# Kernel tuning notes

Hardware: AMD Instinct MI355X
Metric: run time of the kernel (lower is better)

Reference implementation:

```python
import jax, jax.numpy as jnp
import numpy as np

DIM = 512
HEADS = 8
DIM_HEAD = 64
LANDMARKS = 256
PINV_ITERS = 6
RES_K = 33


def layernorm(x, g, b, eps=1e-5):
    mu = jnp.mean(x, -1, keepdims=True)
    var = jnp.mean((x - mu) ** 2, -1, keepdims=True)
    return (x - mu) / jnp.sqrt(var + eps) * g + b


def moore_penrose_pinv(x, iters=PINV_ITERS):
    abs_x = jnp.abs(x)
    col = abs_x.sum(-1)
    row = abs_x.sum(-2)
    z = jnp.swapaxes(x, -1, -2) / (jnp.max(col) * jnp.max(row))
    I = jnp.eye(x.shape[-1], dtype=x.dtype)
    for _ in range(iters):
        xz = x @ z
        z = 0.25 * z @ (13.0 * I - xz @ (15.0 * I - xz @ (7.0 * I - xz)))
    return z


def nystrom_attention(x, Wqkv, Wout, bout, res_w):
    b, n, _ = x.shape
    m = LANDMARKS
    pad = (m - n % m) % m
    if pad:
        x = jnp.pad(x, ((0, 0), (pad, 0), (0, 0)))  # front pad, as in lucidrains impl
    qkv = x @ Wqkv  # (b, np, 3*inner)
    q, k, v = jnp.split(qkv, 3, axis=-1)
    to_heads = lambda t: t.reshape(b, -1, HEADS, DIM_HEAD).transpose(0, 2, 1, 3)
    q, k, v = to_heads(q), to_heads(k), to_heads(v)  # (b,h,np,d)
    q = q * (DIM_HEAD ** -0.5)
    l = -(-n // m)  # ceil(n/m), tokens per landmark
    ql = q.reshape(b, HEADS, m, l, DIM_HEAD).sum(3) / l  # (b,h,m,d)
    kl = k.reshape(b, HEADS, m, l, DIM_HEAD).sum(3) / l
    sim1 = jnp.einsum('bhid,bhjd->bhij', q, kl)   # (b,h,np,m)
    sim2 = jnp.einsum('bhid,bhjd->bhij', ql, kl)  # (b,h,m,m)
    sim3 = jnp.einsum('bhid,bhjd->bhij', ql, k)   # (b,h,m,np)
    a1 = jax.nn.softmax(sim1, -1)
    a2 = jax.nn.softmax(sim2, -1)
    a3 = jax.nn.softmax(sim3, -1)
    a2_inv = moore_penrose_pinv(a2)
    out = (a1 @ a2_inv) @ (a3 @ v)  # (b,h,np,d)
    # depthwise residual conv along sequence (kernel 33x1, groups=heads, no bias)
    res = jax.lax.conv_general_dilated(
        v, res_w, (1, 1), [(RES_K // 2, RES_K // 2), (0, 0)],
        dimension_numbers=('NCHW', 'OIHW', 'NCHW'), feature_group_count=HEADS)
    out = out + res
    out = out.transpose(0, 2, 1, 3).reshape(b, -1, HEADS * DIM_HEAD)
    out = out @ Wout + bout
    return out[:, -n:]


def depthwise2d(x, w, b, pad):
    y = jax.lax.conv_general_dilated(
        x, w, (1, 1), [(pad, pad), (pad, pad)],
        dimension_numbers=('NCHW', 'OIHW', 'NCHW'), feature_group_count=DIM)
    return y + b[None, :, None, None]


def ppeg(x, H, W, w7, b7, w5, b5, w3, b3):
    B, _, C = x.shape
    cls_tok, feat = x[:, :1], x[:, 1:]
    cnn = feat.transpose(0, 2, 1).reshape(B, C, H, W)
    y = depthwise2d(cnn, w7, b7, 3) + cnn + depthwise2d(cnn, w5, b5, 2) + depthwise2d(cnn, w3, b3, 1)
    y = y.reshape(B, C, H * W).transpose(0, 2, 1)
    return jnp.concatenate([cls_tok, y], axis=1)


def setup_inputs() -> dict:
    key = jax.random.key(0)
    ks = jax.random.split(key, 20)
    s = 0.02
    n_classes = 5
    inp = {
        'data': jax.random.normal(ks[0], (1, 15000, 1024), jnp.float32),
        'W_fc1': jax.random.normal(ks[1], (1024, DIM), jnp.float32) * s,
        'b_fc1': jnp.zeros((DIM,), jnp.float32),
        'cls_token': jax.random.normal(ks[2], (1, 1, DIM), jnp.float32),
        'ln1_g': jnp.ones((DIM,), jnp.float32), 'ln1_b': jnp.zeros((DIM,), jnp.float32),
        'qkv1': jax.random.normal(ks[3], (DIM, 3 * HEADS * DIM_HEAD), jnp.float32) * s,
        'out1_w': jax.random.normal(ks[4], (HEADS * DIM_HEAD, DIM), jnp.float32) * s,
        'out1_b': jnp.zeros((DIM,), jnp.float32),
        'res1': jax.random.normal(ks[5], (HEADS, 1, RES_K, 1), jnp.float32) * s,
        'w7': jax.random.normal(ks[6], (DIM, 1, 7, 7), jnp.float32) * s,
        'b7': jnp.zeros((DIM,), jnp.float32),
        'w5': jax.random.normal(ks[7], (DIM, 1, 5, 5), jnp.float32) * s,
        'b5': jnp.zeros((DIM,), jnp.float32),
        'w3': jax.random.normal(ks[8], (DIM, 1, 3, 3), jnp.float32) * s,
        'b3': jnp.zeros((DIM,), jnp.float32),
        'ln2_g': jnp.ones((DIM,), jnp.float32), 'ln2_b': jnp.zeros((DIM,), jnp.float32),
        'qkv2': jax.random.normal(ks[9], (DIM, 3 * HEADS * DIM_HEAD), jnp.float32) * s,
        'out2_w': jax.random.normal(ks[10], (HEADS * DIM_HEAD, DIM), jnp.float32) * s,
        'out2_b': jnp.zeros((DIM,), jnp.float32),
        'res2': jax.random.normal(ks[11], (HEADS, 1, RES_K, 1), jnp.float32) * s,
        'norm_g': jnp.ones((DIM,), jnp.float32), 'norm_b': jnp.zeros((DIM,), jnp.float32),
        'W_fc2': jax.random.normal(ks[12], (DIM, n_classes), jnp.float32) * s,
        'b_fc2': jnp.zeros((n_classes,), jnp.float32),
    }
    return inp


def reference(data, W_fc1, b_fc1, cls_token, ln1_g, ln1_b, qkv1, out1_w, out1_b, res1,
              w7, b7, w5, b5, w3, b3, ln2_g, ln2_b, qkv2, out2_w, out2_b, res2,
              norm_g, norm_b, W_fc2, b_fc2):
    h = jax.nn.relu(data @ W_fc1 + b_fc1)  # (B, N, 512)
    N = h.shape[1]
    _H = int(np.ceil(np.sqrt(N)))
    _W = _H
    add = _H * _W - N
    h = jnp.concatenate([h, h[:, :add]], axis=1)  # pad to square grid
    B = h.shape[0]
    h = jnp.concatenate([jnp.broadcast_to(cls_token, (B, 1, DIM)), h], axis=1)
    h = h + nystrom_attention(layernorm(h, ln1_g, ln1_b), qkv1, out1_w, out1_b, res1)
    h = ppeg(h, _H, _W, w7, b7, w5, b5, w3, b3)
    h = h + nystrom_attention(layernorm(h, ln2_g, ln2_b), qkv2, out2_w, out2_b, res2)
    h = layernorm(h, norm_g, norm_b)[:, 0]
    logits = h @ W_fc2 + b_fc2
    Y_prob = jax.nn.softmax(logits, -1)
    Y_hat = jnp.argmax(logits, -1)
    return logits, Y_prob, Y_hat
```

## Files before the change

kernel.cpp:

```cpp
#include <hip/hip_runtime.h>
#include <math.h>

#define NP 15360
#define NPQ 15488
#define NTOK 15130
#define HG 123

typedef __attribute__((ext_vector_type(8))) short s8b;
typedef __attribute__((ext_vector_type(4))) float f4;

__device__ inline float bf2f(ushort u) { return __uint_as_float(((unsigned)u) << 16); }
__device__ inline ushort f2bf(float f) {
    unsigned u = __float_as_uint(f);
    unsigned r = (u + 0x7fffu + ((u >> 16) & 1u)) >> 16;
    return (ushort)r;
}

__global__ __launch_bounds__(256)
void gemm_f32(const float* __restrict__ A, int lda, long sA,
              const float* __restrict__ B, int ldb, long sB,
              float* __restrict__ C, int ldc, long sC,
              int M, int N, int K,
              const float* __restrict__ bias,
              const float* __restrict__ E, int ldE, long sE, float eS,
              float cS, int relu, int accum)
{
    A += (long)blockIdx.z * sA;
    B += (long)blockIdx.z * sB;
    C += (long)blockIdx.z * sC;
    if (E) E += (long)blockIdx.z * sE;
    const int m0 = blockIdx.y * 64, n0 = blockIdx.x * 64;
    const int t = threadIdx.x;
    const int tx = t & 15, ty = t >> 4;
    __shared__ float As[16][64];
    __shared__ float Bs[16][64];
    float acc[4][4] = {};
    const int arow = t >> 2, akc = (t & 3) * 4;
    const int brow = t >> 4, bnc = (t & 15) * 4;
    for (int k0 = 0; k0 < K; k0 += 16) {
        float4 av = make_float4(0.f, 0.f, 0.f, 0.f);
        if (m0 + arow < M) av = *(const float4*)(A + (long)(m0 + arow) * lda + k0 + akc);
        As[akc + 0][arow] = av.x; As[akc + 1][arow] = av.y;
        As[akc + 2][arow] = av.z; As[akc + 3][arow] = av.w;
        float4 bv = *(const float4*)(B + (long)(k0 + brow) * ldb + n0 + bnc);
        *(float4*)&Bs[brow][bnc] = bv;
        __syncthreads();
#pragma unroll
        for (int kk = 0; kk < 16; ++kk) {
            float4 a4 = *(const float4*)&As[kk][ty * 4];
            float4 b4 = *(const float4*)&Bs[kk][tx * 4];
            float a[4] = {a4.x, a4.y, a4.z, a4.w};
            float b[4] = {b4.x, b4.y, b4.z, b4.w};
#pragma unroll
            for (int i = 0; i < 4; i++)
#pragma unroll
                for (int j = 0; j < 4; j++) acc[i][j] = fmaf(a[i], b[j], acc[i][j]);
        }
        __syncthreads();
    }
#pragma unroll
    for (int i = 0; i < 4; i++) {
        int m = m0 + ty * 4 + i;
        if (m < M) {
#pragma unroll
            for (int j = 0; j < 4; j++) {
                int n = n0 + tx * 4 + j;
                float v = cS * acc[i][j];
                if (E) v = fmaf(eS, E[(long)m * ldE + n], v);
                if (bias) v += bias[n];
                if (relu) v = fmaxf(v, 0.f);
                if (accum) C[(long)m * ldc + n] += v;
                else C[(long)m * ldc + n] = v;
            }
        }
    }
}

template<int MT, int NT, int WROWS, int WCOLS>
__global__ __launch_bounds__(256)
void gemm_mfma(const ushort* __restrict__ A, int lda, long sA,
               const ushort* __restrict__ Bt, int ldb, long sB,
               float* __restrict__ C, int ldc, long sC,
               int M, int K,
               const float* __restrict__ bias, int relu, int accum)
{
    constexpr int TM = MT * 16 * WROWS;
    constexpr int TN = NT * 16 * WCOLS;
    constexpr int BKP = 40;
    constexpr int AIT = TM / 64;
    constexpr int BIT = TN / 64;
    __shared__ ushort As[TM * BKP];
    __shared__ ushort Bs[TN * BKP];
    A  += (long)blockIdx.z * sA;
    Bt += (long)blockIdx.z * sB;
    C  += (long)blockIdx.z * sC;
    const int t = threadIdx.x;
    const int nwg = gridDim.x * gridDim.y;
    const int flat = blockIdx.y * gridDim.x + blockIdx.x;
    const int q8 = nwg >> 3, r8 = nwg & 7;
    const int xcd = flat & 7, idx = flat >> 3;
    const int swz = (xcd < r8) ? (xcd * (q8 + 1) + idx)
                               : (r8 * (q8 + 1) + (xcd - r8) * q8 + idx);
    const int m0 = (swz / gridDim.x) * TM;
    const int n0 = (swz % gridDim.x) * TN;
    const int w = t >> 6, l = t & 63;
    const int wm = (w / WCOLS) * (MT * 16), wn = (w % WCOLS) * (NT * 16);
    const int lr = l & 15;
    const int lk = (l >> 4) * 8;
    const int srow = t >> 2, skc = (t & 3) * 8;
    f4 acc[MT][NT] = {};
    s8b pa[AIT], pb[BIT];
#pragma unroll
    for (int i = 0; i < AIT; i++)
        pa[i] = *(const s8b*)(A + (long)(m0 + srow + i * 64) * lda + skc);
#pragma unroll
    for (int i = 0; i < BIT; i++)
        pb[i] = *(const s8b*)(Bt + (long)(n0 + srow + i * 64) * ldb + skc);
    for (int k0 = 0; k0 < K; k0 += 32) {
        __syncthreads();
#pragma unroll
        for (int i = 0; i < AIT; i++)
            *(s8b*)(&As[(srow + i * 64) * BKP + skc]) = pa[i];
#pragma unroll
        for (int i = 0; i < BIT; i++)
            *(s8b*)(&Bs[(srow + i * 64) * BKP + skc]) = pb[i];
        if (k0 + 32 < K) {
#pragma unroll
            for (int i = 0; i < AIT; i++)
                pa[i] = *(const s8b*)(A + (long)(m0 + srow + i * 64) * lda + k0 + 32 + skc);
#pragma unroll
            for (int i = 0; i < BIT; i++)
                pb[i] = *(const s8b*)(Bt + (long)(n0 + srow + i * 64) * ldb + k0 + 32 + skc);
        }
        __syncthreads();
        s8b af[MT], bf[NT];
#pragma unroll
        for (int i = 0; i < MT; i++) af[i] = *(const s8b*)(&As[(wm + i * 16 + lr) * BKP + lk]);
#pragma unroll
        for (int j = 0; j < NT; j++) bf[j] = *(const s8b*)(&Bs[(wn + j * 16 + lr) * BKP + lk]);
#pragma unroll
        for (int i = 0; i < MT; i++)
#pragma unroll
            for (int j = 0; j < NT; j++)
                acc[i][j] = __builtin_amdgcn_mfma_f32_16x16x32_bf16(af[i], bf[j], acc[i][j], 0, 0, 0);
    }
    const int orow = (l >> 4) * 4;
#pragma unroll
    for (int i = 0; i < MT; i++) {
#pragma unroll
        for (int r = 0; r < 4; r++) {
            int m = m0 + wm + i * 16 + orow + r;
            if (m < M) {
#pragma unroll
                for (int j = 0; j < NT; j++) {
                    int n = n0 + wn + j * 16 + lr;
                    float vv = acc[i][j][r];
                    if (bias) vv += bias[n];
                    if (relu) vv = fmaxf(vv, 0.f);
                    if (accum) C[(long)m * ldc + n] += vv;
                    else C[(long)m * ldc + n] = vv;
                }
            }
        }
    }
}

__global__ __launch_bounds__(256)
void gemm_nn16(const ushort* __restrict__ A, const ushort* __restrict__ B,
               const ushort* __restrict__ E, ushort* __restrict__ C,
               int N, int K, float cS, float eS, long sAB)
{
    __shared__ ushort As[64 * 40];
    __shared__ ushort Bs[64 * 40];
    A += (long)blockIdx.z * sAB;
    B += (long)blockIdx.z * sAB;
    if (E) E += (long)blockIdx.z * sAB;
    C += (long)blockIdx.z * sAB;
    const int t = threadIdx.x;
    const int m0 = blockIdx.y * 64, n0 = blockIdx.x * 64;
    const int w = t >> 6, l = t & 63;
    const int wm = (w >> 1) * 32, wn = (w & 1) * 32;
    const int lr = l & 15, lk = (l >> 4) * 8;
    const int quad = l >> 4;
    const int arow = t >> 2, akc = (t & 3) * 8;
    const int bkk = t >> 3, bnc = (t & 7) * 8;
    const int bcolp = (bkk + ((bnc >> 3) & 3) * 8) & 31;
    f4 acc[2][2] = {};
    s8b pa = *(const s8b*)(A + (long)(m0 + arow) * K + akc);
    s8b pb = *(const s8b*)(B + (long)bkk * N + n0 + bnc);
    for (int k0 = 0; k0 < K; k0 += 32) {
        __syncthreads();
        *(s8b*)(&As[arow * 40 + akc]) = pa;
#pragma unroll
        for (int j = 0; j < 8; j++) Bs[(bnc + j) * 40 + bcolp] = ((ushort*)&pb)[j];
        if (k0 + 32 < K) {
            pa = *(const s8b*)(A + (long)(m0 + arow) * K + k0 + 32 + akc);
            pb = *(const s8b*)(B + (long)(k0 + 32 + bkk) * N + n0 + bnc);
        }
        __syncthreads();
        s8b af[2], bf[2];
#pragma unroll
        for (int i = 0; i < 2; i++) af[i] = *(const s8b*)(&As[(wm + i * 16 + lr) * 40 + lk]);
#pragma unroll
        for (int j = 0; j < 2; j++) {
            int n = wn + j * 16 + lr;
            int cb = ((quad + ((n >> 3) & 3)) & 3) * 8;
            bf[j] = *(const s8b*)(&Bs[n * 40 + cb]);
        }
#pragma unroll
        for (int i = 0; i < 2; i++)
#pragma unroll
            for (int j = 0; j < 2; j++)
                acc[i][j] = __builtin_amdgcn_mfma_f32_16x16x32_bf16(af[i], bf[j], acc[i][j], 0, 0, 0);
    }
    const int orow = (l >> 4) * 4;
#pragma unroll
    for (int i = 0; i < 2; i++)
#pragma unroll
        for (int r = 0; r < 4; r++) {
            int m = m0 + wm + i * 16 + orow + r;
#pragma unroll
            for (int j = 0; j < 2; j++) {
                int n = wn + j * 16 + lr;
                float vv = cS * acc[i][j][r];
                if (E) vv = fmaf(eS, bf2f(E[(long)m * N + n0 + n]), vv);
                C[(long)m * N + n0 + n] = f2bf(vv);
            }
        }
}

__global__ __launch_bounds__(256)
void gemm_qkv_mfma(const ushort* __restrict__ A, const ushort* __restrict__ Bt,
                   ushort* __restrict__ qo, ushort* __restrict__ ko, ushort* __restrict__ vo)
{
    constexpr int BKP = 40;
    __shared__ ushort As[128 * BKP];
    __shared__ ushort Bs[128 * BKP];
    const int t = threadIdx.x;
    const int nwg = gridDim.x * gridDim.y;
    const int flat = blockIdx.y * gridDim.x + blockIdx.x;
    const int q8 = nwg >> 3, r8 = nwg & 7;
    const int xcd = flat & 7, idx = flat >> 3;
    const int swz = (xcd < r8) ? (xcd * (q8 + 1) + idx)
                               : (r8 * (q8 + 1) + (xcd - r8) * q8 + idx);
    const int m0 = (swz / gridDim.x) * 128;
    const int n0 = (swz % gridDim.x) * 128;
    const int w = t >> 6, l = t & 63;
    const int wm = (w >> 1) * 64, wn = (w & 1) * 64;
    const int lr = l & 15;
    const int lk = (l >> 4) * 8;
    const int srow = t >> 2, skc = (t & 3) * 8;
    f4 acc[4][4] = {};
    s8b pa[2], pb[2];
#pragma unroll
    for (int i = 0; i < 2; i++) {
        pa[i] = *(const s8b*)(A + (long)(m0 + srow + i * 64) * 512 + skc);
        pb[i] = *(const s8b*)(Bt + (long)(n0 + srow + i * 64) * 512 + skc);
    }
    for (int k0 = 0; k0 < 512; k0 += 32) {
        __syncthreads();
#pragma unroll
        for (int i = 0; i < 2; i++) {
            *(s8b*)(&As[(srow + i * 64) * BKP + skc]) = pa[i];
            *(s8b*)(&Bs[(srow + i * 64) * BKP + skc]) = pb[i];
        }
        if (k0 + 32 < 512) {
#pragma unroll
            for (int i = 0; i < 2; i++) {
                pa[i] = *(const s8b*)(A + (long)(m0 + srow + i * 64) * 512 + k0 + 32 + skc);
                pb[i] = *(const s8b*)(Bt + (long)(n0 + srow + i * 64) * 512 + k0 + 32 + skc);
            }
        }
        __syncthreads();
        s8b af[4], bf[4];
#pragma unroll
        for (int i = 0; i < 4; i++) af[i] = *(const s8b*)(&As[(wm + i * 16 + lr) * BKP + lk]);
#pragma unroll
        for (int j = 0; j < 4; j++) bf[j] = *(const s8b*)(&Bs[(wn + j * 16 + lr) * BKP + lk]);
#pragma unroll
        for (int i = 0; i < 4; i++)
#pragma unroll
            for (int j = 0; j < 4; j++)
                acc[i][j] = __builtin_amdgcn_mfma_f32_16x16x32_bf16(af[i], bf[j], acc[i][j], 0, 0, 0);
    }
    const int orow = (l >> 4) * 4;
#pragma unroll
    for (int i = 0; i < 4; i++) {
#pragma unroll
        for (int r = 0; r < 4; r++) {
            int m = m0 + wm + i * 16 + orow + r;
#pragma unroll
            for (int j = 0; j < 4; j++) {
                int col = n0 + wn + j * 16 + lr;
                int which = col >> 9, h = (col >> 6) & 7, d = col & 63;
                float vv = acc[i][j][r];
                if (which == 0) vv *= 0.125f;
                ushort* dst = which == 0 ? qo : (which == 1 ? ko : vo);
                dst[((long)h * NPQ + m) * 64 + d] = f2bf(vv);
            }
        }
    }
}

__global__ __launch_bounds__(256, 3)
void k_flash_a3v(const ushort* __restrict__ qlb, const ushort* __restrict__ kg,
                 const ushort* __restrict__ vg,
                 float* __restrict__ pacc, float* __restrict__ pml)
{
    const int c = blockIdx.x;
    const int qt = blockIdx.y;
    const int h = blockIdx.z;
    const int t = threadIdx.x;
    const int w = t >> 6, lane = t & 63;
    const int quad = lane >> 4, l16 = lane & 15;
    const s8b vones = {0x3F80, 0x3F80, 0x3F80, 0x3F80, 0x3F80, 0x3F80, 0x3F80, 0x3F80};

    __shared__ union {
        struct { ushort Vt[64][40]; ushort Ps[128][40]; } s;
        float Os[128][68];
    } L;

    s8b aq[2][2];
    const ushort* qbase = qlb + ((long)h * 256 + qt * 128 + w * 32) * 64;
#pragma unroll
    for (int mi = 0; mi < 2; mi++)
#pragma unroll
        for (int kf = 0; kf < 2; kf++)
            aq[mi][kf] = *(const s8b*)(qbase + (mi * 16 + l16) * 64 + kf * 32 + quad * 8);

    f4 oacc[2][4] = {};
    f4 lacc[2] = {};

    const ushort* kh = kg + (long)h * NPQ * 64;
    const ushort* vh = vg + (long)h * NPQ * 64;
    const int key0c = c * 256;

    const int vkk = (t >> 3) & 31;
    const int vdc = (t & 7) * 8;
    const int vcolp = (vkk + ((vdc >> 3) & 3) * 8) & 31;

    s8b vvN = *(const s8b*)(vh + (long)(key0c + vkk) * 64 + vdc);
    s8b bqN[2][2];
#pragma unroll
    for (int nj = 0; nj < 2; nj++)
#pragma unroll
        for (int kf = 0; kf < 2; kf++)
            bqN[nj][kf] = *(const s8b*)(kh + (long)(key0c + nj * 16 + l16) * 64 + kf * 32 + quad * 8);

#pragma unroll
    for (int sub = 0; sub < 8; sub++) {
        int key0 = key0c + sub * 32;
        s8b vvC = vvN;
        s8b bq[2][2];
#pragma unroll
        for (int nj = 0; nj < 2; nj++)
#pragma unroll
            for (int kf = 0; kf < 2; kf++) bq[nj][kf] = bqN[nj][kf];
        if (sub < 7) {
            vvN = *(const s8b*)(vh + (long)(key0 + 32 + vkk) * 64 + vdc);
#pragma unroll
            for (int nj = 0; nj < 2; nj++)
#pragma unroll
                for (int kf = 0; kf < 2; kf++)
                    bqN[nj][kf] = *(const s8b*)(kh + (long)(key0 + 32 + nj * 16 + l16) * 64 + kf * 32 + quad * 8);
        }
        __syncthreads();
        {
#pragma unroll
            for (int j = 0; j < 8; j++) L.s.Vt[vdc + j][vcolp] = ((ushort*)&vvC)[j];
        }
        f4 sacc[2][2] = {};
#pragma unroll
        for (int mi = 0; mi < 2; mi++)
#pragma unroll
            for (int nj = 0; nj < 2; nj++) {
                sacc[mi][nj] = __builtin_amdgcn_mfma_f32_16x16x32_bf16(aq[mi][0], bq[nj][0], sacc[mi][nj], 0, 0, 0);
                sacc[mi][nj] = __builtin_amdgcn_mfma_f32_16x16x32_bf16(aq[mi][1], bq[nj][1], sacc[mi][nj], 0, 0, 0);
            }
#pragma unroll
        for (int mi = 0; mi < 2; mi++)
#pragma unroll
            for (int r = 0; r < 4; r++) {
                int row = w * 32 + mi * 16 + quad * 4 + r;
                L.s.Ps[row][l16]      = f2bf(__expf(sacc[mi][0][r]));
                L.s.Ps[row][16 + l16] = f2bf(__expf(sacc[mi][1][r]));
            }
        __syncthreads();
        s8b ap[2], bv[4];
#pragma unroll
        for (int mi = 0; mi < 2; mi++)
            ap[mi] = *(const s8b*)(&L.s.Ps[w * 32 + mi * 16 + l16][quad * 8]);
#pragma unroll
        for (int dj = 0; dj < 4; dj++) {
            int d = dj * 16 + l16;
            int rot = (d >> 3) & 3;
            int cb = ((quad + rot) & 3) * 8;
            bv[dj] = *(const s8b*)(&L.s.Vt[d][cb]);
        }
#pragma unroll
        for (int mi = 0; mi < 2; mi++) {
#pragma unroll
            for (int dj = 0; dj < 4; dj++)
                oacc[mi][dj] = __builtin_amdgcn_mfma_f32_16x16x32_bf16(ap[mi], bv[dj], oacc[mi][dj], 0, 0, 0);
            lacc[mi] = __builtin_amdgcn_mfma_f32_16x16x32_bf16(ap[mi], vones, lacc[mi], 0, 0, 0);
        }
    }
    __syncthreads();
#pragma unroll
    for (int mi = 0; mi < 2; mi++)
#pragma unroll
        for (int dj = 0; dj < 4; dj++)
#pragma unroll
            for (int r = 0; r < 4; r++)
                L.Os[w * 32 + mi * 16 + quad * 4 + r][dj * 16 + l16] = oacc[mi][dj][r];
    long pbase = (long)(h * 60 + c);
    if (l16 == 0) {
#pragma unroll
        for (int mi = 0; mi < 2; mi++)
#pragma unroll
            for (int r = 0; r < 4; r++) {
                int i = qt * 128 + w * 32 + mi * 16 + quad * 4 + r;
                pml[pbase * 512 + i] = 0.f;
                pml[pbase * 512 + 256 + i] = lacc[mi][r];
            }
    }
    __syncthreads();
    float* pc = pacc + pbase * 16384 + qt * 128;
    int d = t >> 2, ig = t & 3;
#pragma unroll
    for (int u = 0; u < 8; u++) {
        int i0 = ig * 32 + u * 4;
        float4 v4 = make_float4(L.Os[i0][d], L.Os[i0 + 1][d], L.Os[i0 + 2][d], L.Os[i0 + 3][d]);
        *(float4*)(pc + (long)d * 256 + i0) = v4;
    }
}

__global__ __launch_bounds__(256, 3)
void k_attn1(const ushort* __restrict__ qg, const ushort* __restrict__ klb,
             const ushort* __restrict__ BmT, const ushort* __restrict__ vg,
             const float* __restrict__ rw, ushort* __restrict__ ohb)
{
    const int m0 = blockIdx.x * 128;
    const int h = blockIdx.y;
    const int t = threadIdx.x;
    const int w = t >> 6, lane = t & 63;
    const int quad = lane >> 4, l16 = lane & 15;
    const s8b vones = {0x3F80, 0x3F80, 0x3F80, 0x3F80, 0x3F80, 0x3F80, 0x3F80, 0x3F80};

    __shared__ union {
        ushort Ps[2][128][40];
        ushort Os[128][68];
    } L;
    __shared__ __attribute__((aligned(16))) ushort Vs[160][64];

    const ushort* vh = vg + (long)h * NPQ * 64;
    {
        const ushort* srcw = vh + (long)(214 + m0 + w * 40) * 64 + lane * 8;
        ushort* dstw = &Vs[w * 40][0];
#pragma unroll
        for (int it = 0; it < 5; it++)
            __builtin_amdgcn_global_load_lds(
                (const __attribute__((address_space(1))) void*)(srcw + it * 512),
                (__attribute__((address_space(3))) void*)(dstw + it * 512),
                16, 0, 0);
    }

    s8b aq[2][2];
    const ushort* qbase = qg + ((long)h * NPQ + 230 + m0 + w * 32) * 64;
#pragma unroll
    for (int mi = 0; mi < 2; mi++)
#pragma unroll
        for (int kf = 0; kf < 2; kf++)
            aq[mi][kf] = *(const s8b*)(qbase + (mi * 16 + l16) * 64 + kf * 32 + quad * 8);

    const ushort* kh = klb + (long)h * 16384;
    const ushort* bmt = BmT + (long)h * 16384;

    s8b bqN[2][2];
#pragma unroll
    for (int nj = 0; nj < 2; nj++)
#pragma unroll
        for (int kf = 0; kf < 2; kf++)
            bqN[nj][kf] = *(const s8b*)(kh + (long)(nj * 16 + l16) * 64 + kf * 32 + quad * 8);

    f4 oacc[2][4] = {};
    f4 lacc[2] = {};
#pragma unroll
    for (int sub = 0; sub < 8; sub++) {
        int key0 = sub * 32;
        s8b bq[2][2];
#pragma unroll
        for (int nj = 0; nj < 2; nj++)
#pragma unroll
            for (int kf = 0; kf < 2; kf++) bq[nj][kf] = bqN[nj][kf];
        if (sub < 7) {
#pragma unroll
            for (int nj = 0; nj < 2; nj++)
#pragma unroll
                for (int kf = 0; kf < 2; kf++)
                    bqN[nj][kf] = *(const s8b*)(kh + (long)(key0 + 32 + nj * 16 + l16) * 64 + kf * 32 + quad * 8);
        }
        s8b bv[4];
#pragma unroll
        for (int dj = 0; dj < 4; dj++)
            bv[dj] = *(const s8b*)(bmt + (long)(dj * 16 + l16) * 256 + key0 + quad * 8);
        f4 sacc[2][2] = {};
#pragma unroll
        for (int mi = 0; mi < 2; mi++)
#pragma unroll
            for (int nj = 0; nj < 2; nj++) {
                sacc[mi][nj] = __builtin_amdgcn_mfma_f32_16x16x32_bf16(aq[mi][0], bq[nj][0], sacc[mi][nj], 0, 0, 0);
                sacc[mi][nj] = __builtin_amdgcn_mfma_f32_16x16x32_bf16(aq[mi][1], bq[nj][1], sacc[mi][nj], 0, 0, 0);
            }
        int par = sub & 1;
#pragma unroll
        for (int mi = 0; mi < 2; mi++)
#pragma unroll
            for (int r = 0; r < 4; r++) {
                int row = w * 32 + mi * 16 + quad * 4 + r;
                L.Ps[par][row][l16]      = f2bf(__expf(sacc[mi][0][r]));
                L.Ps[par][row][16 + l16] = f2bf(__expf(sacc[mi][1][r]));
            }
        s8b ap[2];
#pragma unroll
        for (int mi = 0; mi < 2; mi++)
            ap[mi] = *(const s8b*)(&L.Ps[par][w * 32 + mi * 16 + l16][quad * 8]);
#pragma unroll
        for (int mi = 0; mi < 2; mi++) {
#pragma unroll
            for (int dj = 0; dj < 4; dj++)
                oacc[mi][dj] = __builtin_amdgcn_mfma_f32_16x16x32_bf16(ap[mi], bv[dj], oacc[mi][dj], 0, 0, 0);
            lacc[mi] = __builtin_amdgcn_mfma_f32_16x16x32_bf16(ap[mi], vones, lacc[mi], 0, 0, 0);
        }
    }
    __syncthreads();

    if (214 + m0 + 160 > NP) {
        for (int r = w * 32; r < w * 32 + 64 && r < 160; ++r)
            if (214 + m0 + r >= NP) Vs[r][lane] = 0;
    }

#pragma unroll
    for (int mi = 0; mi < 2; mi++)
#pragma unroll
        for (int r = 0; r < 4; r++) {
            float inv = 1.f / lacc[mi][r];
            int row = w * 32 + mi * 16 + quad * 4 + r;
#pragma unroll
            for (int dj = 0; dj < 4; dj++)
                L.Os[row][dj * 16 + l16] = f2bf(oacc[mi][dj][r] * inv);
        }
    float rwf[33];
#pragma unroll
    for (int kk = 0; kk < 33; kk++) rwf[kk] = rw[h * 33 + kk];
#pragma unroll
    for (int half = 0; half < 2; half++) {
        const int rbase = w * 32 + half * 16;
        float vr[48];
#pragma unroll
        for (int s = 0; s < 48; s++) vr[s] = bf2f(Vs[rbase + s][lane]);
        float conv[16];
#pragma unroll
        for (int i = 0; i < 16; i++) conv[i] = 0.f;
#pragma unroll
        for (int kk = 0; kk < 33; kk++) {
            float wk = rwf[kk];
#pragma unroll
            for (int i = 0; i < 16; i++) conv[i] = fmaf(wk, vr[i + kk], conv[i]);
        }
        int t0 = m0 + rbase;
#pragma unroll
        for (int i = 0; i < 16; i++) {
            int tk = t0 + i;
            if (tk < NTOK) {
                float val = bf2f(L.Os[rbase + i][lane]) + conv[i];
                ohb[(long)tk * 512 + h * 64 + lane] = f2bf(val);
            }
        }
    }
}

__global__ __launch_bounds__(256)
void k_layernorm(const float* __restrict__ h, ushort* __restrict__ xln,
                 const float* __restrict__ g, const float* __restrict__ b, int pad)
{
    int row = blockIdx.x, t = threadIdx.x;
    if (row < pad) {
        xln[(long)row * 512 + t] = 0;
        xln[(long)row * 512 + t + 256] = 0;
        return;
    }
    const float* src = h + (long)(row - pad) * 512;
    float x1 = src[t], x2 = src[t + 256];
    float s = x1 + x2, q = x1 * x1 + x2 * x2;
    __shared__ float rs[4], rq[4], st[2];
    int wid = t >> 6, lane = t & 63;
#pragma unroll
    for (int o = 32; o > 0; o >>= 1) { s += __shfl_down(s, o); q += __shfl_down(q, o); }
    if (lane == 0) { rs[wid] = s; rq[wid] = q; }
    __syncthreads();
    if (t == 0) {
        float S = rs[0] + rs[1] + rs[2] + rs[3];
        float Q = rq[0] + rq[1] + rq[2] + rq[3];
        float mean = S / 512.f;
        float var = Q / 512.f - mean * mean;
        st[0] = mean; st[1] = rsqrtf(var + 1e-5f);
    }
    __syncthreads();
    float mean = st[0], rstd = st[1];
    xln[(long)row * 512 + t] = f2bf((x1 - mean) * rstd * g[t] + b[t]);
    xln[(long)row * 512 + t + 256] = f2bf((x2 - mean) * rstd * g[t + 256] + b[t + 256]);
}

__global__ __launch_bounds__(256)
void k_padcls(float* __restrict__ hbuf, const float* __restrict__ cls)
{
    int i = blockIdx.x, t = threadIdx.x;
    if (i == 0) { hbuf[t] = cls[t]; hbuf[t + 256] = cls[t + 256]; }
    else {
        hbuf[(long)(15000 + i) * 512 + t] = hbuf[(long)i * 512 + t];
        hbuf[(long)(15000 + i) * 512 + t + 256] = hbuf[(long)i * 512 + t + 256];
    }
}

__global__ __launch_bounds__(256)
void k_wT(const float* __restrict__ Wm, ushort* __restrict__ Wt, int K, int N, long sW, long sWt)
{
    Wm += (long)blockIdx.z * sW; Wt += (long)blockIdx.z * sWt;
    __shared__ float tile[32][33];
    int tx = threadIdx.x & 31, ty = threadIdx.x >> 5;
    int n0 = blockIdx.x * 32, k0 = blockIdx.y * 32;
#pragma unroll
    for (int u = 0; u < 4; u++) tile[ty + u * 8][tx] = Wm[(long)(k0 + ty + u * 8) * N + n0 + tx];
    __syncthreads();
#pragma unroll
    for (int u = 0; u < 4; u++) Wt[(long)(n0 + ty + u * 8) * K + k0 + tx] = f2bf(tile[tx][ty + u * 8]);
}

__global__ __launch_bounds__(256)
void k_cvt(const float4* __restrict__ src, ushort4* __restrict__ dst, long n4)
{
    long i = (long)blockIdx.x * 256 + threadIdx.x;
    if (i < n4) {
        float4 v = src[i];
        ushort4 o;
        o.x = f2bf(v.x); o.y = f2bf(v.y); o.z = f2bf(v.z); o.w = f2bf(v.w);
        dst[i] = o;
    }
}

__global__ __launch_bounds__(256)
void k_b2f(const ushort4* __restrict__ src, float4* __restrict__ dst, long n4)
{
    long i = (long)blockIdx.x * 256 + threadIdx.x;
    if (i < n4) {
        ushort4 v = src[i];
        dst[i] = make_float4(bf2f(v.x), bf2f(v.y), bf2f(v.z), bf2f(v.w));
    }
}

__global__ __launch_bounds__(64)
void k_landmarks(const ushort* __restrict__ q, const ushort* __restrict__ k,
                 float* __restrict__ ql, ushort* __restrict__ qlb,
                 float* __restrict__ klT, ushort* __restrict__ klb,
                 unsigned* __restrict__ scal)
{
    int i = blockIdx.x, h = blockIdx.y, d = threadIdx.x;
    if (i == 0 && h == 0 && d == 0) { scal[0] = 0u; scal[1] = 0u; }
    long base = ((long)h * NPQ + (long)i * 60) * 64 + d;
    float sq = 0.f, sk = 0.f;
    for (int j = 0; j < 60; j++) { sq += bf2f(q[base + j * 64]); sk += bf2f(k[base + j * 64]); }
    float qv = sq / 60.f, kv = sk / 60.f;
    ql[((long)h * 256 + i) * 64 + d] = qv;
    qlb[((long)h * 256 + i) * 64 + d] = f2bf(qv);
    klT[((long)h * 64 + d) * 256 + i] = kv;
    klb[((long)h * 256 + i) * 64 + d] = f2bf(kv);
}

__global__ __launch_bounds__(256)
void k_softmax256(float* __restrict__ X, ushort* __restrict__ X16, long headStride)
{
    float* row = X + (long)blockIdx.y * headStride + (long)blockIdx.x * 256;
    int t = threadIdx.x, wid = t >> 6, lane = t & 63;
    float x = row[t];
    __shared__ float rm[4], rsum[4], fin[2];
    float m = x;
#pragma unroll
    for (int o = 32; o > 0; o >>= 1) m = fmaxf(m, __shfl_down(m, o));
    if (lane == 0) rm[wid] = m;
    __syncthreads();
    if (t == 0) fin[0] = fmaxf(fmaxf(rm[0], rm[1]), fmaxf(rm[2], rm[3]));
    __syncthreads();
    float e = __expf(x - fin[0]);
    float s = e;
#pragma unroll
    for (int o = 32; o > 0; o >>= 1) s += __shfl_down(s, o);
    if (lane == 0) rsum[wid] = s;
    __syncthreads();
    if (t == 0) fin[1] = rsum[0] + rsum[1] + rsum[2] + rsum[3];
    __syncthreads();
    float v = e / fin[1];
    row[t] = v;
    if (X16) X16[(long)blockIdx.y * headStride + (long)blockIdx.x * 256 + t] = f2bf(v);
}

__global__ __launch_bounds__(256)
void k_colmax(const float* __restrict__ a2, unsigned* __restrict__ scal)
{
    int h = blockIdx.x, t = threadIdx.x, wid = t >> 6, lane = t & 63;
    const float* A = a2 + (long)h * 65536;
    float cs = 0.f, rs = 0.f;
    for (int i = 0; i < 256; i++) cs += A[(long)i * 256 + t];
    for (int j = 0; j < 256; j++) rs += A[(long)t * 256 + j];
    __shared__ float r1[4], r2[4];
    float m1v = cs, m2v = rs;
#pragma unroll
    for (int o = 32; o > 0; o >>= 1) {
        m1v = fmaxf(m1v, __shfl_down(m1v, o));
        m2v = fmaxf(m2v, __shfl_down(m2v, o));
    }
    if (lane == 0) { r1[wid] = m1v; r2[wid] = m2v; }
    __syncthreads();
    if (t == 0) {
        float a = fmaxf(fmaxf(r1[0], r1[1]), fmaxf(r1[2], r1[3]));
        float b = fmaxf(fmaxf(r2[0], r2[1]), fmaxf(r2[2], r2[3]));
        atomicMax(scal + 0, __float_as_uint(a));
        atomicMax(scal + 1, __float_as_uint(b));
    }
}

__global__ __launch_bounds__(256)
void k_zinit(const float* __restrict__ a2, ushort* __restrict__ zb, const unsigned* __restrict__ scal)
{
    float s = 1.f / (__uint_as_float(scal[0]) * __uint_as_float(scal[1]));
    const float* A = a2 + (long)blockIdx.z * 65536;
    ushort* Z = zb + (long)blockIdx.z * 65536;
    __shared__ float tile[32][33];
    int tx = threadIdx.x & 31, ty = threadIdx.x >> 5;
    int i0 = blockIdx.x * 32, j0 = blockIdx.y * 32;
#pragma unroll
    for (int u = 0; u < 4; u++) tile[ty + u * 8][tx] = A[(long)(j0 + ty + u * 8) * 256 + i0 + tx];
    __syncthreads();
#pragma unroll
    for (int u = 0; u < 4; u++) Z[(long)(i0 + ty + u * 8) * 256 + j0 + tx] = f2bf(tile[tx][ty + u * 8] * s);
}

__global__ __launch_bounds__(256)
void k_a3v_merge(const float* __restrict__ pacc, const float* __restrict__ pml,
                 float* __restrict__ t1)
{
    int d = blockIdx.x, h = blockIdx.y, i = threadIdx.x;
    float M = -INFINITY, L = 0.f, num = 0.f;
    for (int c = 0; c < 60; c++) {
        float mc = pml[(long)(h * 60 + c) * 2 * 256 + i];
        float lc = pml[((long)(h * 60 + c) * 2 + 1) * 256 + i];
        float ac = pacc[((long)(h * 60 + c) * 64 + d) * 256 + i];
        if (mc > M) {
            float f = __expf(M - mc);
            num = num * f + ac; L = L * f + lc; M = mc;
        } else {
            float p = __expf(mc - M);
            num = fmaf(p, ac, num); L = fmaf(p, lc, L);
        }
    }
    t1[((long)h * 256 + i) * 64 + d] = num / L;
}

__global__ __launch_bounds__(256)
void k_cls(const ushort* __restrict__ qb, const float* __restrict__ klT,
           const float* __restrict__ Bm, const ushort* __restrict__ vb,
           const float* __restrict__ rw, float* __restrict__ oh)
{
    int h = blockIdx.x, t = threadIdx.x, wid = t >> 6, lane = t & 63;
    __shared__ float qs[64], p[256], red[256];
    __shared__ float rm[4], rsum[4], fin[2];
    if (t < 64) qs[t] = bf2f(qb[((long)h * NPQ + 230) * 64 + t]);
    __syncthreads();
    float s = 0.f;
    for (int d = 0; d < 64; d++) s = fmaf(qs[d], klT[((long)h * 64 + d) * 256 + t], s);
    float m = s;
#pragma unroll
    for (int o = 32; o > 0; o >>= 1) m = fmaxf(m, __shfl_down(m, o));
    if (lane == 0) rm[wid] = m;
    __syncthreads();
    if (t == 0) fin[0] = fmaxf(fmaxf(rm[0], rm[1]), fmaxf(rm[2], rm[3]));
    __syncthreads();
    float e = __expf(s - fin[0]);
    float ss = e;
#pragma unroll
    for (int o = 32; o > 0; o >>= 1) ss += __shfl_down(ss, o);
    if (lane == 0) rsum[wid] = ss;
    __syncthreads();
    if (t == 0) fin[1] = rsum[0] + rsum[1] + rsum[2] + rsum[3];
    __syncthreads();
    p[t] = e / fin[1];
    __syncthreads();
    int d = t & 63, grp = t >> 6;
    float o = 0.f;
    for (int j = grp * 64; j < grp * 64 + 64; j++) o = fmaf(p[j], Bm[((long)h * 256 + j) * 64 + d], o);
    red[t] = o;
    __syncthreads();
    if (t < 64) {
        float val = red[t] + red[t + 64] + red[t + 128] + red[t + 192];
#pragma unroll
        for (int kk = 0; kk < 33; kk++)
            val = fmaf(rw[h * 33 + kk], bf2f(vb[((long)h * NPQ + 214 + kk) * 64 + t]), val);
        oh[h * 64 + t] = val;
    }
}

__global__ __launch_bounds__(256)
void k_copy4(const float4* __restrict__ src, float4* __restrict__ dst, long n4)
{
    long i = (long)blockIdx.x * 256 + threadIdx.x;
    if (i < n4) dst[i] = src[i];
}

__global__ __launch_bounds__(512)
void k_wcomb(const float* __restrict__ w7, const float* __restrict__ b7,
             const float* __restrict__ w5, const float* __restrict__ b5,
             const float* __restrict__ w3, const float* __restrict__ b3,
             float* __restrict__ wc, float* __restrict__ bc)
{
    int k = blockIdx.x, c = threadIdx.x;
    int kr = k / 7, kc = k % 7;
    float v = w7[c * 49 + k];
    if (kr >= 1 && kr <= 5 && kc >= 1 && kc <= 5) v += w5[c * 25 + (kr - 1) * 5 + (kc - 1)];
    if (kr >= 2 && kr <= 4 && kc >= 2 && kc <= 4) v += w3[c * 9 + (kr - 2) * 3 + (kc - 2)];
    if (k == 24) v += 1.f;
    wc[k * 512 + c] = v;
    if (k == 0) bc[c] = b7[c] + b5[c] + b3[c];
}

__global__ __launch_bounds__(256, 4)
void k_ppeg4(const float* __restrict__ cnn, float* __restrict__ hbuf,
             const float* __restrict__ wc, const float* __restrict__ bc)
{
    __shared__ __attribute__((aligned(16))) float tile[320 * 32];
    const int t = threadIdx.x;
    const int w = t >> 6, lane = t & 63;
    const int c0 = blockIdx.x * 16;
    const int r0 = blockIdx.y * 8;
    const int cb = blockIdx.z * 32;
    {
        const int pl = lane >> 3;
        const int c4 = (lane & 7) * 4;
#pragma unroll
        for (int it = 0; it < 10; ++it) {
            int chunk = w * 10 + it;
            int pos = chunk * 8 + pl;
            int pr = pos / 22, pc = pos - pr * 22;
            int gr = r0 + pr - 3, gc = c0 + pc - 3;
            int grc = min(max(gr, 0), HG - 1), gcc = min(max(gc, 0), HG - 1);
            const float* src = cnn + (long)(grc * HG + gcc) * 512 + cb + c4;
            __builtin_amdgcn_global_load_lds(
                (const __attribute__((address_space(1))) void*)src,
                (__attribute__((address_space(3))) void*)(tile + chunk * 256),
                16, 0, 0);
        }
    }
    __syncthreads();
    const bool boundary = (r0 < 3) | (r0 > HG - 11) | (c0 < 3) | (c0 > HG - 19);
    if (boundary) {
        for (int pos = t; pos < 308; pos += 256) {
            int pr = pos / 22, pc = pos - pr * 22;
            int gr = r0 + pr - 3, gc = c0 + pc - 3;
            if (gr < 0 || gr >= HG || gc < 0 || gc >= HG) {
                float4 z = make_float4(0.f, 0.f, 0.f, 0.f);
#pragma unroll
                for (int c4 = 0; c4 < 32; c4 += 4) *(float4*)&tile[pos * 32 + c4] = z;
            }
        }
        __syncthreads();
    }
    const int cp = t & 15;
    const int slot = t >> 4;
    const int orow = slot >> 1;
    const int ohalf = (slot & 1) * 8;
    float a0[8], a1[8];
#pragma unroll
    for (int i = 0; i < 8; i++) { a0[i] = 0.f; a1[i] = 0.f; }
    for (int kr = 0; kr < 7; kr++) {
        float w0[14], w1[14];
        const float* trow = tile + ((orow + kr) * 22 + ohalf) * 32 + cp * 2;
#pragma unroll
        for (int j = 0; j < 14; j++) {
            float2 v = *(const float2*)(trow + j * 32);
            w0[j] = v.x; w1[j] = v.y;
        }
#pragma unroll
        for (int kc = 0; kc < 7; kc++) {
            float2 wv = *(const float2*)(wc + (long)(kr * 7 + kc) * 512 + cb + cp * 2);
#pragma unroll
            for (int i = 0; i < 8; i++) {
                a0[i] = fmaf(wv.x, w0[i + kc], a0[i]);
                a1[i] = fmaf(wv.y, w1[i + kc], a1[i]);
            }
        }
    }
    const float2 bv = *(const float2*)(bc + cb + cp * 2);
    const int gr = r0 + orow;
    if (gr < HG) {
#pragma unroll
        for (int i = 0; i < 8; i++) {
            int gc = c0 + ohalf + i;
            if (gc < HG) {
                float* dst = hbuf + (long)(1 + gr * HG + gc) * 512 + cb + cp * 2;
                dst[0] = a0[i] + bv.x;
                dst[1] = a1[i] + bv.y;
            }
        }
    }
}

__global__ __launch_bounds__(256)
void k_final(const float* __restrict__ hbuf, const float* __restrict__ g,
             const float* __restrict__ b, const float* __restrict__ W2,
             const float* __restrict__ b2, float* __restrict__ out)
{
    __shared__ float y[512];
    __shared__ float rs[4], rq[4], st[2], lg[8];
    int t = threadIdx.x, wid = t >> 6, lane = t & 63;
    float x1 = hbuf[t], x2 = hbuf[t + 256];
    float s = x1 + x2, q = x1 * x1 + x2 * x2;
#pragma unroll
    for (int o = 32; o > 0; o >>= 1) { s += __shfl_down(s, o); q += __shfl_down(q, o); }
    if (lane == 0) { rs[wid] = s; rq[wid] = q; }
    __syncthreads();
    if (t == 0) {
        float S = rs[0] + rs[1] + rs[2] + rs[3];
        float Q = rq[0] + rq[1] + rq[2] + rq[3];
        float mean = S / 512.f;
        float var = Q / 512.f - mean * mean;
        st[0] = mean; st[1] = rsqrtf(var + 1e-5f);
    }
    __syncthreads();
    float mean = st[0], rstd = st[1];
    y[t] = (x1 - mean) * rstd * g[t] + b[t];
    y[t + 256] = (x2 - mean) * rstd * g[t + 256] + b[t + 256];
    __syncthreads();
    if (t < 5) {
        float acc = b2[t];
        for (int kx = 0; kx < 512; kx++) acc = fmaf(y[kx], W2[kx * 5 + t], acc);
        lg[t] = acc;
    }
    __syncthreads();
    if (t == 0) {
        float mx = lg[0]; int am = 0;
        for (int j = 1; j < 5; j++) if (lg[j] > mx) { mx = lg[j]; am = j; }
        float e[5], se = 0.f;
        for (int j = 0; j < 5; j++) { e[j] = __expf(lg[j] - mx); se += e[j]; }
        for (int j = 0; j < 5; j++) { out[j] = lg[j]; out[5 + j] = e[j] / se; }
        out[10] = (float)am;
    }
}

extern "C" void kernel_launch(void* const* d_in, const int* in_sizes, int n_in,
                              void* d_out, int out_size, void* d_ws, size_t ws_size,
                              hipStream_t stream)
{
    const float* data  = (const float*)d_in[0];
    const float* Wfc1  = (const float*)d_in[1];
    const float* bfc1  = (const float*)d_in[2];
    const float* cls   = (const float*)d_in[3];
    const float* ln1g  = (const float*)d_in[4];
    const float* ln1b  = (const float*)d_in[5];
    const float* qkv1  = (const float*)d_in[6];
    const float* out1w = (const float*)d_in[7];
    const float* out1b = (const float*)d_in[8];
    const float* res1  = (const float*)d_in[9];
    const float* w7    = (const float*)d_in[10];
    const float* b7    = (const float*)d_in[11];
    const float* w5    = (const float*)d_in[12];
    const float* b5    = (const float*)d_in[13];
    const float* w3    = (const float*)d_in[14];
    const float* b3    = (const float*)d_in[15];
    const float* ln2g  = (const float*)d_in[16];
    const float* ln2b  = (const float*)d_in[17];
    const float* qkv2  = (const float*)d_in[18];
    const float* out2w = (const float*)d_in[19];
    const float* out2b = (const float*)d_in[20];
    const float* res2  = (const float*)d_in[21];
    const float* normg = (const float*)d_in[22];
    const float* normb = (const float*)d_in[23];
    const float* Wfc2  = (const float*)d_in[24];
    const float* bfc2  = (const float*)d_in[25];
    float* out = (float*)d_out;

    float* W = (float*)d_ws;
    size_t off = 0;
    auto alloc = [&](size_t n) { size_t o = off; off += (n + 255) & ~(size_t)255; return o; };
    float*  hbuf   = W + alloc((size_t)NTOK * 512);
    float*  ohreg  = W + alloc((size_t)15232 * 512);
    float*  oh     = ohreg;
    ushort* xln    = (ushort*)ohreg;
    ushort* qb16   = (ushort*)(W + alloc((size_t)8 * NPQ * 32));
    ushort* kb16   = (ushort*)(W + alloc((size_t)8 * NPQ * 32));
    ushort* vb16   = (ushort*)(W + alloc((size_t)8 * NPQ * 32));
    float*  ql     = W + alloc(8 * 256 * 64);
    ushort* qlb    = (ushort*)(W + alloc(8 * 256 * 32));
    float*  klT    = W + alloc(8 * 64 * 256);
    ushort* klb    = (ushort*)(W + alloc(8 * 256 * 32));
    float*  a2     = W + alloc(8 * 65536);
    ushort* a2b    = (ushort*)(W + alloc(8 * 32768));
    ushort* zb0    = (ushort*)(W + alloc(8 * 32768));
    ushort* zb1    = (ushort*)(W + alloc(8 * 32768));
    ushort* m1b    = (ushort*)(W + alloc(8 * 32768));
    ushort* mab    = (ushort*)(W + alloc(8 * 32768));
    ushort* mbb    = (ushort*)(W + alloc(8 * 32768));
    float*  z0     = W + alloc(8 * 65536);
    float*  t1     = W + alloc(8 * 256 * 64);
    float*  Bm     = W + alloc(8 * 256 * 64);
    ushort* BmbT   = (ushort*)(W + alloc(8 * 256 * 32));
    float*  scal   = W + alloc(64);
    ushort* ohb16  = (ushort*)(W + alloc((size_t)15232 * 256));
    ushort* WfcT   = (ushort*)(W + alloc(1024 * 256));
    ushort* qkv1T  = (ushort*)(W + alloc(1536 * 256));
    ushort* qkv2T  = (ushort*)(W + alloc(1536 * 256));
    ushort* out1T  = (ushort*)(W + alloc(512 * 256));
    ushort* out2T  = (ushort*)(W + alloc(512 * 256));
    float*  wc     = W + alloc(49 * 512);
    float*  bc     = W + alloc(512);
    float*  big    = W + alloc(8110080);
    ushort* datab  = (ushort*)big;
    float*  pacc   = big;
    float*  pml    = big + 7864320;
    float*  cnn    = big;
    if (ws_size < off * sizeof(float)) return;

    k_wT<<<dim3(16, 32, 1), 256, 0, stream>>>(Wfc1, WfcT, 1024, 512, 0, 0);
    k_wT<<<dim3(48, 16, 1), 256, 0, stream>>>(qkv1, qkv1T, 512, 1536, 0, 0);
    k_wT<<<dim3(48, 16, 1), 256, 0, stream>>>(qkv2, qkv2T, 512, 1536, 0, 0);
    k_wT<<<dim3(16, 16, 1), 256, 0, stream>>>(out1w, out1T, 512, 512, 0, 0);
    k_wT<<<dim3(16, 16, 1), 256, 0, stream>>>(out2w, out2T, 512, 512, 0, 0);
    k_wcomb<<<49, 512, 0, stream>>>(w7, b7, w5, b5, w3, b3, wc, bc);
    k_cvt<<<15000, 256, 0, stream>>>((const float4*)data, (ushort4*)datab, 3840000);
    gemm_mfma<2, 4, 2, 2><<<dim3(4, 235, 1), 256, 0, stream>>>(
        datab, 1024, 0, WfcT, 1024, 0, hbuf + 512, 512, 0, 15000, 1024, bfc1, 1, 0);
    k_padcls<<<130, 256, 0, stream>>>(hbuf, cls);

    auto layer = [&](const float* lng, const float* lnb, const ushort* qkvT,
                     const float* outW, const ushort* outT, const float* outB,
                     const float* resW, bool full) {
        k_layernorm<<<NP, 256, 0, stream>>>(hbuf, xln, lng, lnb, 230);
        gemm_qkv_mfma<<<dim3(12, 120, 1), 256, 0, stream>>>(xln, qkvT, qb16, kb16, vb16);
        k_landmarks<<<dim3(256, 8), 64, 0, stream>>>(qb16, kb16, ql, qlb, klT, klb, (unsigned*)scal);
        gemm_f32<<<dim3(4, 4, 8), 256, 0, stream>>>(ql, 64, 16384, klT, 256, 16384,
            a2, 256, 65536, 256, 256, 64, nullptr, nullptr, 0, 0, 0.f, 1.f, 0, 0);
        k_softmax256<<<dim3(256, 8), 256, 0, stream>>>(a2, a2b, 65536);
        k_colmax<<<8, 256, 0, stream>>>(a2, (unsigned*)scal);
        k_zinit<<<dim3(8, 8, 8), 256, 0, stream>>>(a2, zb0, (const unsigned*)scal);
        ushort* zbi = zb0; ushort* zbo = zb1;
        for (int it = 0; it < 6; ++it) {
            gemm_nn16<<<dim3(4, 4, 8), 256, 0, stream>>>(a2b, zbi, nullptr, m1b, 256, 256, 1.f, 0.f, 65536);
            gemm_nn16<<<dim3(4, 4, 8), 256, 0, stream>>>(m1b, m1b, m1b, mab, 256, 256, -1.f, 7.f, 65536);
            gemm_nn16<<<dim3(4, 4, 8), 256, 0, stream>>>(m1b, mab, m1b, mbb, 256, 256, -1.f, 15.f, 65536);
            gemm_nn16<<<dim3(4, 4, 8), 256, 0, stream>>>(zbi, mbb, zbi, zbo, 256, 256, -0.25f, 3.25f, 65536);
            ushort* tmp = zbi; zbi = zbo; zbo = tmp;
        }
        k_b2f<<<512, 256, 0, stream>>>((const ushort4*)zbi, (float4*)z0, 131072);
        k_flash_a3v<<<dim3(60, 2, 8), 256, 0, stream>>>(qlb, kb16, vb16, pacc, pml);
        k_a3v_merge<<<dim3(64, 8), 256, 0, stream>>>(pacc, pml, t1);
        gemm_f32<<<dim3(1, 4, 8), 256, 0, stream>>>(z0, 256, 65536, t1, 64, 16384,
            Bm, 64, 16384, 256, 64, 256, nullptr, nullptr, 0, 0, 0.f, 1.f, 0, 0);
        if (full) {
            k_wT<<<dim3(2, 8, 8), 256, 0, stream>>>(Bm, BmbT, 256, 64, 16384, 16384);
            k_attn1<<<dim3(119, 8), 256, 0, stream>>>(qb16, klb, BmbT, vb16, resW, ohb16);
            gemm_mfma<2, 4, 2, 2><<<dim3(4, 237, 1), 256, 0, stream>>>(
                ohb16, 512, 0, outT, 512, 0, hbuf, 512, 0, NTOK, 512, outB, 0, 1);
        } else {
            k_cls<<<8, 256, 0, stream>>>(qb16, klT, Bm, vb16, resW, oh);
            gemm_f32<<<dim3(8, 1, 1), 256, 0, stream>>>(oh, 512, 0, outW, 512, 0,
                hbuf, 512, 0, 1, 512, 512, outB, nullptr, 0, 0, 0.f, 1.f, 0, 1);
        }
    };

    layer(ln1g, ln1b, qkv1T, out1w, out1T, out1b, res1, true);
    k_copy4<<<(1936512 + 255) / 256, 256, 0, stream>>>((const float4*)(hbuf + 512), (float4*)cnn, 1936512);
    k_ppeg4<<<dim3(8, 16, 16), 256, 0, stream>>>(cnn, hbuf, wc, bc);
    layer(ln2g, ln2b, qkv2T, out2w, out2T, out2b, res2, false);
    k_final<<<1, 256, 0, stream>>>(hbuf, normg, normb, Wfc2, bfc2, out);
}
```

Baseline: 1.027 ms.

## Fuse pinv iteration GEMM launches into one persistent kernel with grid barriers

Replaces the 24 separate small bf16 GEMM launches of the Newton-Schulz pseudo-inverse loop with a single persistent 128-block kernel. Stages are separated by a global atomic counter barrier, and the counter is reset in k_zinit. This removes per-launch overhead and gaps between many tiny kernels. It relies on all 128 blocks being co-resident and adds spin-wait barrier cost. After an even number of iterations the final z lands back in zb0, which the conversion reads.

```diff
diff --git a/kernel.cpp b/kernel.cpp
--- a/kernel.cpp
+++ b/kernel.cpp
@@ -165,19 +165,82 @@
     }
 }
 
-__global__ __launch_bounds__(256)
-void gemm_nn16(const ushort* __restrict__ A, const ushort* __restrict__ B,
-               const ushort* __restrict__ E, ushort* __restrict__ C,
-               int N, int K, float cS, float eS, long sAB)
+__device__ __forceinline__ void gbar(unsigned* cnt, unsigned target)
+{
+    __syncthreads();
+    __threadfence();
+    if (threadIdx.x == 0) {
+        __hip_atomic_fetch_add(cnt, 1u, __ATOMIC_RELEASE, __HIP_MEMORY_SCOPE_AGENT);
+        while (__hip_atomic_load(cnt, __ATOMIC_ACQUIRE, __HIP_MEMORY_SCOPE_AGENT) < target)
+            __builtin_amdgcn_s_sleep(4);
+    }
+    __syncthreads();
+    __threadfence();
+}
+
+__device__ __forceinline__ void pv_stage(
+    const ushort* __restrict__ A, const ushort* __restrict__ B,
+    const ushort* __restrict__ E, ushort* __restrict__ C,
+    float cS, float eS, ushort* As, ushort* Bs,
+    int m0, int n0, int wm, int wn, int lr, int lk, int quad,
+    int arow, int akc, int bkk, int bnc, int bcolp, int orow)
+{
+    f4 acc[2][2] = {};
+    s8b pa = *(const s8b*)(A + (long)(m0 + arow) * 256 + akc);
+    s8b pb = *(const s8b*)(B + (long)bkk * 256 + n0 + bnc);
+    for (int k0 = 0; k0 < 256; k0 += 32) {
+        __syncthreads();
+        *(s8b*)(&As[arow * 40 + akc]) = pa;
+#pragma unroll
+        for (int j = 0; j < 8; j++) Bs[(bnc + j) * 40 + bcolp] = ((ushort*)&pb)[j];
+        if (k0 + 32 < 256) {
+            pa = *(const s8b*)(A + (long)(m0 + arow) * 256 + k0 + 32 + akc);
+            pb = *(const s8b*)(B + (long)(k0 + 32 + bkk) * 256 + n0 + bnc);
+        }
+        __syncthreads();
+        s8b af[2], bf[2];
+#pragma unroll
+        for (int i = 0; i < 2; i++) af[i] = *(const s8b*)(&As[(wm + i * 16 + lr) * 40 + lk]);
+#pragma unroll
+        for (int j = 0; j < 2; j++) {
+            int n = wn + j * 16 + lr;
+            int cb = ((quad + ((n >> 3) & 3)) & 3) * 8;
+            bf[j] = *(const s8b*)(&Bs[n * 40 + cb]);
+        }
+#pragma unroll
+        for (int i = 0; i < 2; i++)
+#pragma unroll
+            for (int j = 0; j < 2; j++)
+                acc[i][j] = __builtin_amdgcn_mfma_f32_16x16x32_bf16(af[i], bf[j], acc[i][j], 0, 0, 0);
+    }
+#pragma unroll
+    for (int i = 0; i < 2; i++)
+#pragma unroll
+        for (int r = 0; r < 4; r++) {
+            int m = m0 + wm + i * 16 + orow + r;
+#pragma unroll
+            for (int j = 0; j < 2; j++) {
+                int n = wn + j * 16 + lr;
+                float vv = cS * acc[i][j][r];
+                if (E) vv = fmaf(eS, bf2f(E[(long)m * 256 + n0 + n]), vv);
+                C[(long)m * 256 + n0 + n] = f2bf(vv);
+            }
+        }
+}
+
+__global__ __launch_bounds__(256)
+void k_pinv2(const ushort* __restrict__ a2b, ushort* __restrict__ z0,
+             ushort* __restrict__ z1, ushort* __restrict__ m1,
+             ushort* __restrict__ ma, ushort* __restrict__ mb,
+             unsigned* __restrict__ cnt)
 {
     __shared__ ushort As[64 * 40];
     __shared__ ushort Bs[64 * 40];
-    A += (long)blockIdx.z * sAB;
-    B += (long)blockIdx.z * sAB;
-    if (E) E += (long)blockIdx.z * sAB;
-    C += (long)blockIdx.z * sAB;
+    const int bid = blockIdx.x;
+    const long hs = (long)(bid >> 4) * 65536;
+    const int m0 = ((bid >> 2) & 3) * 64;
+    const int n0 = (bid & 3) * 64;
     const int t = threadIdx.x;
-    const int m0 = blockIdx.y * 64, n0 = blockIdx.x * 64;
     const int w = t >> 6, l = t & 63;
     const int wm = (w >> 1) * 32, wn = (w & 1) * 32;
     const int lr = l & 15, lk = (l >> 4) * 8;
@@ -185,48 +248,25 @@
     const int arow = t >> 2, akc = (t & 3) * 8;
     const int bkk = t >> 3, bnc = (t & 7) * 8;
     const int bcolp = (bkk + ((bnc >> 3) & 3) * 8) & 31;
-    f4 acc[2][2] = {};
-    s8b pa = *(const s8b*)(A + (long)(m0 + arow) * K + akc);
-    s8b pb = *(const s8b*)(B + (long)bkk * N + n0 + bnc);
-    for (int k0 = 0; k0 < K; k0 += 32) {
-        __syncthreads();
-        *(s8b*)(&As[arow * 40 + akc]) = pa;
-#pragma unroll
-        for (int j = 0; j < 8; j++) Bs[(bnc + j) * 40 + bcolp] = ((ushort*)&pb)[j];
-        if (k0 + 32 < K) {
-            pa = *(const s8b*)(A + (long)(m0 + arow) * K + k0 + 32 + akc);
-            pb = *(const s8b*)(B + (long)(k0 + 32 + bkk) * N + n0 + bnc);
-        }
-        __syncthreads();
-        s8b af[2], bf[2];
-#pragma unroll
-        for (int i = 0; i < 2; i++) af[i] = *(const s8b*)(&As[(wm + i * 16 + lr) * 40 + lk]);
-#pragma unroll
-        for (int j = 0; j < 2; j++) {
-            int n = wn + j * 16 + lr;
-            int cb = ((quad + ((n >> 3) & 3)) & 3) * 8;
-            bf[j] = *(const s8b*)(&Bs[n * 40 + cb]);
-        }
-#pragma unroll
-        for (int i = 0; i < 2; i++)
-#pragma unroll
-            for (int j = 0; j < 2; j++)
-                acc[i][j] = __builtin_amdgcn_mfma_f32_16x16x32_bf16(af[i], bf[j], acc[i][j], 0, 0, 0);
-    }
     const int orow = (l >> 4) * 4;
-#pragma unroll
-    for (int i = 0; i < 2; i++)
-#pragma unroll
-        for (int r = 0; r < 4; r++) {
-            int m = m0 + wm + i * 16 + orow + r;
-#pragma unroll
-            for (int j = 0; j < 2; j++) {
-                int n = wn + j * 16 + lr;
-                float vv = cS * acc[i][j][r];
-                if (E) vv = fmaf(eS, bf2f(E[(long)m * N + n0 + n]), vv);
-                C[(long)m * N + n0 + n] = f2bf(vv);
-            }
-        }
+    const ushort* A2 = a2b + hs;
+    ushort* zin  = z0 + hs;
+    ushort* zout = z1 + hs;
+    ushort* M1 = m1 + hs;
+    ushort* MA = ma + hs;
+    ushort* MB = mb + hs;
+    unsigned bar = 0;
+    for (int it = 0; it < 6; ++it) {
+        pv_stage(A2,  zin, nullptr, M1,   1.f,   0.f,  As, Bs, m0, n0, wm, wn, lr, lk, quad, arow, akc, bkk, bnc, bcolp, orow);
+        gbar(cnt, (++bar) * 128u);
+        pv_stage(M1,  M1,  M1,     MA,   -1.f,   7.f,  As, Bs, m0, n0, wm, wn, lr, lk, quad, arow, akc, bkk, bnc, bcolp, orow);
+        gbar(cnt, (++bar) * 128u);
+        pv_stage(M1,  MA,  M1,     MB,   -1.f,  15.f,  As, Bs, m0, n0, wm, wn, lr, lk, quad, arow, akc, bkk, bnc, bcolp, orow);
+        gbar(cnt, (++bar) * 128u);
+        pv_stage(zin, MB,  zin,    zout, -0.25f, 3.25f, As, Bs, m0, n0, wm, wn, lr, lk, quad, arow, akc, bkk, bnc, bcolp, orow);
+        if (it < 5) gbar(cnt, (++bar) * 128u);
+        ushort* tmp = zin; zin = zout; zout = tmp;
+    }
 }
 
 __global__ __launch_bounds__(256)
@@ -730,8 +770,11 @@
 }
 
 __global__ __launch_bounds__(256)
-void k_zinit(const float* __restrict__ a2, ushort* __restrict__ zb, const unsigned* __restrict__ scal)
-{
+void k_zinit(const float* __restrict__ a2, ushort* __restrict__ zb,
+             const unsigned* __restrict__ scal, unsigned* __restrict__ cnt)
+{
+    if (blockIdx.x == 0 && blockIdx.y == 0 && blockIdx.z == 0 && threadIdx.x == 0)
+        cnt[0] = 0u;
     float s = 1.f / (__uint_as_float(scal[0]) * __uint_as_float(scal[1]));
     const float* A = a2 + (long)blockIdx.z * 65536;
     ushort* Z = zb + (long)blockIdx.z * 65536;
@@ -1027,6 +1070,7 @@
     float*  pml    = big + 7864320;
     float*  cnn    = big;
     if (ws_size < off * sizeof(float)) return;
+    unsigned* pcnt = (unsigned*)scal + 8;
 
     k_wT<<<dim3(16, 32, 1), 256, 0, stream>>>(Wfc1, WfcT, 1024, 512, 0, 0);
     k_wT<<<dim3(48, 16, 1), 256, 0, stream>>>(qkv1, qkv1T, 512, 1536, 0, 0);
@@ -1049,16 +1093,9 @@
             a2, 256, 65536, 256, 256, 64, nullptr, nullptr, 0, 0, 0.f, 1.f, 0, 0);
         k_softmax256<<<dim3(256, 8), 256, 0, stream>>>(a2, a2b, 65536);
         k_colmax<<<8, 256, 0, stream>>>(a2, (unsigned*)scal);
-        k_zinit<<<dim3(8, 8, 8), 256, 0, stream>>>(a2, zb0, (const unsigned*)scal);
-        ushort* zbi = zb0; ushort* zbo = zb1;
-        for (int it = 0; it < 6; ++it) {
-            gemm_nn16<<<dim3(4, 4, 8), 256, 0, stream>>>(a2b, zbi, nullptr, m1b, 256, 256, 1.f, 0.f, 65536);
-            gemm_nn16<<<dim3(4, 4, 8), 256, 0, stream>>>(m1b, m1b, m1b, mab, 256, 256, -1.f, 7.f, 65536);
-            gemm_nn16<<<dim3(4, 4, 8), 256, 0, stream>>>(m1b, mab, m1b, mbb, 256, 256, -1.f, 15.f, 65536);
-            gemm_nn16<<<dim3(4, 4, 8), 256, 0, stream>>>(zbi, mbb, zbi, zbo, 256, 256, -0.25f, 3.25f, 65536);
-            ushort* tmp = zbi; zbi = zbo; zbo = tmp;
-        }
-        k_b2f<<<512, 256, 0, stream>>>((const ushort4*)zbi, (float4*)z0, 131072);
+        k_zinit<<<dim3(8, 8, 8), 256, 0, stream>>>(a2, zb0, (const unsigned*)scal, pcnt);
+        k_pinv2<<<128, 256, 0, stream>>>(a2b, zb0, zb1, m1b, mab, mbb, pcnt);
+        k_b2f<<<512, 256, 0, stream>>>((const ushort4*)zb0, (float4*)z0, 131072);
         k_flash_a3v<<<dim3(60, 2, 8), 256, 0, stream>>>(qlb, kb16, vb16, pacc, pml);
         k_a3v_merge<<<dim3(64, 8), 256, 0, stream>>>(pacc, pml, t1);
         gemm_f32<<<dim3(1, 4, 8), 256, 0, stream>>>(z0, 256, 65536, t1, 64, 16384,
```

Result: slower. 2.149 ms (+109.3%).
